# Optimization experiments

Measured on AMD Instinct MI355X. Metric: run time of the kernel, lower is better.

The kernel has to match this reference:

```python
import jax, jax.numpy as jnp
import numpy as np

N, E, H, EF, NG = 50000, 600000, 128, 4, 20
R_MIN, R_MAX = 0.0, 10.0

def setup_inputs() -> dict:
    key = jax.random.key(0)
    ks = jax.random.split(key, 20)
    s = lambda fi, fo: 1.0 / np.sqrt(fi)
    inp = {
        'h': jax.random.normal(ks[0], (N, H), jnp.float32),
        'x': jax.random.normal(ks[1], (N, 3), jnp.float32),
        'edge_index': jax.random.randint(ks[2], (2, E), 0, N, jnp.int32),
        'mask_ligand': jnp.ones((N,), jnp.float32),
        'edge_attr': jax.random.normal(ks[3], (E, EF), jnp.float32),
        # edge_mlp: Linear(2H+EF+NG,H) silu Linear(H,H) silu
        'We1': jax.random.normal(ks[4], (2*H+EF+NG, H), jnp.float32) * s(2*H+EF+NG, H),
        'be1': jnp.zeros((H,), jnp.float32),
        'We2': jax.random.normal(ks[5], (H, H), jnp.float32) * s(H, H),
        'be2': jnp.zeros((H,), jnp.float32),
        # edge_inf: Linear(H,1) sigmoid
        'Winf': jax.random.normal(ks[6], (H, 1), jnp.float32) * s(H, 1),
        'binf': jnp.zeros((1,), jnp.float32),
        # x_mlp: Linear(H,H) silu Linear(H,1,no bias, gain 0.001) tanh
        'Wx1': jax.random.normal(ks[7], (H, H), jnp.float32) * s(H, H),
        'bx1': jnp.zeros((H,), jnp.float32),
        'Wx2': jax.random.normal(ks[8], (H, 1), jnp.float32) * (0.001 * s(H, 1)),
        # node_mlp: Linear(2H,H) silu Linear(H,H)
        'Wn1': jax.random.normal(ks[9], (2*H, H), jnp.float32) * s(2*H, H),
        'bn1': jnp.zeros((H,), jnp.float32),
        'Wn2': jax.random.normal(ks[10], (H, H), jnp.float32) * s(H, H),
        'bn2': jnp.zeros((H,), jnp.float32),
    }
    return inp

def _gaussian_smearing(d):
    # d: [E,1] -> [E,NG]
    offset = jnp.linspace(R_MIN, R_MAX, NG, dtype=d.dtype)
    coeff = -0.5 / (offset[1] - offset[0]) ** 2
    return jnp.exp(coeff * (d - offset) ** 2)

def reference(h, x, edge_index, mask_ligand, edge_attr,
              We1, be1, We2, be2, Winf, binf, Wx1, bx1, Wx2,
              Wn1, bn1, Wn2, bn2):
    src, dst = edge_index[0], edge_index[1]
    hi, hj = h[dst], h[src]                      # [E,H]
    rel_x = x[dst] - x[src]                      # [E,3]
    d_sq = jnp.sum(rel_x ** 2, -1, keepdims=True)  # [E,1]
    d = jnp.sqrt(d_sq + 1e-8)
    d_feat = _gaussian_smearing(d)               # [E,NG]
    edge_feat = jnp.concatenate([d_feat, edge_attr], -1)
    inp = jnp.concatenate([hi, hj, edge_feat], -1)  # [E,2H+NG+EF]
    mij = jax.nn.silu(jax.nn.silu(inp @ We1 + be1) @ We2 + be2)  # [E,H]
    eij = jax.nn.sigmoid(mij @ Winf + binf)       # [E,1]
    n = h.shape[0]
    mi = jax.ops.segment_sum(mij * eij, dst, num_segments=n)  # [N,H]
    h_new = h + (jax.nn.silu(jnp.concatenate([mi, h], -1) @ Wn1 + bn1) @ Wn2 + bn2)
    gate = jnp.tanh(jax.nn.silu(mij @ Wx1 + bx1) @ Wx2)        # [E,1]
    delta_x = jax.ops.segment_sum(rel_x / (d + 1.0) * gate, dst, num_segments=n)
    x_new = x + delta_x * mask_ligand[:, None]
    return h_new, x_new
```

## Files before the change

### kernel.cpp

```cpp
#include <hip/hip_runtime.h>
#include <hip/hip_bf16.h>
#include <cstdint>

#define NN 50000
#define NE 600000
#define HD 128
#define NG 20
#define EF 4
#define K1 280
#define TILES (NE/64)
#define EGRID 512
#define ROWU 148
#define NTILE 782
#define SW(r) ((r) ^ (((r)>>3)&7))
#define EDW 12

typedef __attribute__((ext_vector_type(4))) float f32x4;
typedef __attribute__((ext_vector_type(8))) __bf16 bf16x8;
typedef __attribute__((ext_vector_type(4))) unsigned int u32x4;

__device__ __forceinline__ float fast_rcp(float x){ return __builtin_amdgcn_rcpf(x); }
__device__ __forceinline__ float silu_f(float x){ return x * fast_rcp(1.0f + __expf(-x)); }
__device__ __forceinline__ float sigmoid_f(float x){ return fast_rcp(1.0f + __expf(-x)); }
__device__ __forceinline__ float tanh_f(float x){ return 1.0f - 2.0f*fast_rcp(__expf(2.0f*x)+1.0f); }

__device__ __forceinline__ uint32_t pk2(float a, float b){
  uint32_t ua = __float_as_uint(a); ua += 0x7FFFu + ((ua>>16)&1u);
  uint32_t ub = __float_as_uint(b); ub += 0x7FFFu + ((ub>>16)&1u);
  return (ua>>16) | (ub & 0xFFFF0000u);
}
__device__ __forceinline__ uint16_t bfb(float a){
  uint32_t ua = __float_as_uint(a); ua += 0x7FFFu + ((ua>>16)&1u);
  return (uint16_t)(ua>>16);
}
__device__ __forceinline__ float bf2f(uint16_t b){ return __uint_as_float(((uint32_t)b)<<16); }
__device__ __forceinline__ f32x4 MF(u32x4 a, u32x4 b, f32x4 c){
  return __builtin_amdgcn_mfma_f32_16x16x32_bf16(
      __builtin_bit_cast(bf16x8, a), __builtin_bit_cast(bf16x8, b), c, 0, 0, 0);
}
__device__ __forceinline__ int mf_idx(int r, int c){
  return (((r>>4)*4 + (c>>5))*64 + SW(((((c>>4)&1)<<1) + ((c>>3)&1))*16 + (r&15)))*8 + (c&7);
}

__global__ void __launch_bounds__(256) h2bf_kernel(
    const float* __restrict__ h, uint32_t* __restrict__ hb)
{
  const size_t i = ((size_t)blockIdx.x*256 + threadIdx.x)*8;
  const float4 a = *reinterpret_cast<const float4*>(h + i);
  const float4 b = *reinterpret_cast<const float4*>(h + i + 4);
  u32x4 v = {pk2(a.x,a.y), pk2(a.z,a.w), pk2(b.x,b.y), pk2(b.z,b.w)};
  *reinterpret_cast<u32x4*>(hb + i/2) = v;
}

__global__ void __launch_bounds__(512) hist_kernel(
    const int* __restrict__ ei, int* __restrict__ cnt)
{
  const int e = blockIdx.x*512 + threadIdx.x;
  if (e < NE) atomicAdd(&cnt[ei[NE + e]], 1);
}

__global__ void __launch_bounds__(512) scanA_kernel(
    int* __restrict__ cur, int* __restrict__ bsums)
{
  __shared__ int s[512];
  const int tid = threadIdx.x;
  const int i = blockIdx.x*512 + tid;
  const int v = (i < NN) ? cur[i] : 0;
  s[tid] = v; __syncthreads();
  #pragma unroll
  for (int d = 1; d < 512; d <<= 1){
    const int t = (tid >= d) ? s[tid-d] : 0;
    __syncthreads();
    s[tid] += t;
    __syncthreads();
  }
  if (i < NN) cur[i] = s[tid] - v;
  if (tid == 511) bsums[blockIdx.x] = s[511];
}

__global__ void scanB_kernel(int* __restrict__ bsums)
{
  if (threadIdx.x == 0 && blockIdx.x == 0){
    int acc = 0;
    for (int b = 0; b < 98; ++b){ const int t = bsums[b]; bsums[b] = acc; acc += t; }
  }
}

__global__ void __launch_bounds__(512) scanC_kernel(
    int* __restrict__ cur, const int* __restrict__ bsums)
{
  const int i = blockIdx.x*512 + threadIdx.x;
  if (i < NN) cur[i] += bsums[blockIdx.x];
}

__global__ void __launch_bounds__(512) fill_kernel(
    const int* __restrict__ ei, int* __restrict__ cur, int* __restrict__ perm)
{
  const int e = blockIdx.x*512 + threadIdx.x;
  if (e < NE){
    const int p = atomicAdd(&cur[ei[NE + e]], 1);
    perm[p] = e;
  }
}

__global__ void __launch_bounds__(256) pregather_kernel(
    const int* __restrict__ ei, const float* __restrict__ x,
    const float* __restrict__ eattr, const int* __restrict__ perm,
    uint32_t* __restrict__ edata)
{
  const int i = blockIdx.x*256 + threadIdx.x;
  if (i >= NE) return;
  const int e = perm[i];
  const int sj = ei[e], dj = ei[NE + e];
  const float ax = x[dj*3+0]-x[sj*3+0];
  const float ay = x[dj*3+1]-x[sj*3+1];
  const float az = x[dj*3+2]-x[sj*3+2];
  const float dd = sqrtf(ax*ax + ay*ay + az*az + 1e-8f);
  const float4 e4 = *reinterpret_cast<const float4*>(eattr + (size_t)e*EF);
  uint32_t* dp = edata + (size_t)i*EDW;
  u32x4 v0 = {(uint32_t)sj, (uint32_t)dj, __float_as_uint(ax), __float_as_uint(ay)};
  u32x4 v1 = {__float_as_uint(az), __float_as_uint(dd), __float_as_uint(e4.x), __float_as_uint(e4.y)};
  u32x4 v2 = {__float_as_uint(e4.z), __float_as_uint(e4.w), 0u, 0u};
  *reinterpret_cast<u32x4*>(dp)     = v0;
  *reinterpret_cast<u32x4*>(dp + 4) = v1;
  *reinterpret_cast<u32x4*>(dp + 8) = v2;
}

#define EDGE_LDS_U32 (64*ROWU + 4096 + 4096 + 704)
#define EDGE_LDS_B (EDGE_LDS_U32*4)

__global__ void __launch_bounds__(512, 4) edge_red_kernel(
    const uint32_t* __restrict__ hb, const uint32_t* __restrict__ edata,
    const float* __restrict__ We1, const float* __restrict__ be1,
    const float* __restrict__ We2, const float* __restrict__ be2,
    const float* __restrict__ Winf, const float* __restrict__ binf,
    const float* __restrict__ Wx1, const float* __restrict__ bx1,
    const float* __restrict__ Wx2, float* __restrict__ out)
{
  extern __shared__ uint32_t smem[];
  uint32_t* s_inp = smem;
  uint16_t* t1f   = (uint16_t*)(smem + 64*ROWU);
  uint16_t* mf_   = (uint16_t*)(smem + 64*ROWU + 4096);
  uint32_t* tl    = smem + 64*ROWU + 8192;
  int*   s_dst    = (int*)tl;
  float* s_rel    = (float*)(tl+64);
  float* s_dist   = (float*)(tl+256);
  float* s_pe     = (float*)(tl+320);
  float* s_pg     = (float*)(tl+384);
  int*   s_udst   = (int*)(tl+448);
  int*   s_ustart = (int*)(tl+512);
  int*   s_Un     = (int*)(tl+580);

  const int tid = threadIdx.x;
  const int w = tid >> 6, l = tid & 63;
  const int lo = l & 15, hi = l >> 4;
  const int col = w*16 + lo;
  const int r8 = tid >> 3, p8 = tid & 7;
  const int ks2 = w >> 1;
  const int lp  = ((w&1)*2 + (lo>>3))*16 + 4*hi;
  const int jj  = lo & 7;
  const int lsw = SW(l);

  u32x4 B1[9], B2[4], B3[4];
  #pragma unroll
  for (int ks = 0; ks < 9; ++ks){
    float f[8];
    #pragma unroll
    for (int j = 0; j < 8; ++j){
      const int k = ks*32 + hi*8 + j;
      f[j] = (k < K1) ? We1[k*HD + col] : 0.0f;
    }
    B1[ks] = {pk2(f[0],f[1]), pk2(f[2],f[3]), pk2(f[4],f[5]), pk2(f[6],f[7])};
  }
  #pragma unroll
  for (int ks = 0; ks < 4; ++ks){
    float f2[8], f3[8];
    #pragma unroll
    for (int j = 0; j < 8; ++j){
      const int k = ks*32 + hi*8 + j;
      f2[j] = We2[k*HD + col];
      f3[j] = Wx1[k*HD + col];
    }
    B2[ks] = {pk2(f2[0],f2[1]), pk2(f2[2],f2[3]), pk2(f2[4],f2[5]), pk2(f2[6],f2[7])};
    B3[ks] = {pk2(f3[0],f3[1]), pk2(f3[2],f3[3]), pk2(f3[4],f3[5]), pk2(f3[6],f3[7])};
  }
  const float vbe1 = be1[col], vbe2 = be2[col], vbx1 = bx1[col];
  const float wi = Winf[col], wx = Wx2[col], vbinf = binf[0];
  const float SP = 10.0f/19.0f;
  const float CO = -0.5f/(SP*SP);

  for (int t = blockIdx.x; t < TILES; t += EGRID){
    const int ebase = t*64;
    __syncthreads();

    if (tid < 64){
      const uint32_t* ed = edata + (size_t)(ebase + tid)*EDW;
      const u32x4 w0 = *reinterpret_cast<const u32x4*>(ed);
      const u32x4 w1 = *reinterpret_cast<const u32x4*>(ed + 4);
      const u32x4 w2 = *reinterpret_cast<const u32x4*>(ed + 8);
      const int dj   = (int)w0.y;
      const float ax = __uint_as_float(w0.z);
      const float ay = __uint_as_float(w0.w);
      const float az = __uint_as_float(w1.x);
      const float dd = __uint_as_float(w1.y);
      s_dst[tid] = dj;
      s_rel[3*tid+0]=ax; s_rel[3*tid+1]=ay; s_rel[3*tid+2]=az;
      s_dist[tid]=dd; s_pe[tid]=0.0f; s_pg[tid]=0.0f;
      const int dprev = __shfl_up(dj, 1);
      const int isnew = (tid == 0) || (dj != dprev);
      const unsigned long long mball = __ballot(isnew);
      const int slot = __popcll(mball << (63 - tid)) - 1;
      if (isnew){ s_udst[slot] = dj; s_ustart[slot] = tid; }
      if (tid == 63){ s_Un[0] = slot + 1; s_ustart[slot + 1] = 64; }
      float g[24];
      #pragma unroll
      for (int j = 0; j < 20; ++j){ const float a = dd - j*SP; g[j] = __expf(CO*a*a); }
      g[20]=__uint_as_float(w1.z); g[21]=__uint_as_float(w1.w);
      g[22]=__uint_as_float(w2.x); g[23]=__uint_as_float(w2.y);
      uint32_t* gp = s_inp + tid*ROWU + 128;
      u32x4 g0v = {pk2(g[0],g[1]),  pk2(g[2],g[3]),  pk2(g[4],g[5]),  pk2(g[6],g[7])};
      u32x4 g1v = {pk2(g[8],g[9]),  pk2(g[10],g[11]),pk2(g[12],g[13]),pk2(g[14],g[15])};
      u32x4 g2v = {pk2(g[16],g[17]),pk2(g[18],g[19]),pk2(g[20],g[21]),pk2(g[22],g[23])};
      u32x4 g3v = {0,0,0,0};
      *reinterpret_cast<u32x4*>(gp)    = g0v;
      *reinterpret_cast<u32x4*>(gp+4)  = g1v;
      *reinterpret_cast<u32x4*>(gp+8)  = g2v;
      *reinterpret_cast<u32x4*>(gp+12) = g3v;
    }
    {
      const uint32_t node = edata[(size_t)(ebase + r8)*EDW + (p8 < 4 ? 1 : 0)];
      const uint32_t* hw = hb + (size_t)node*(HD/2) + (p8&3)*16;
      uint32_t* dp = s_inp + r8*ROWU + p8*16;
      #pragma unroll
      for (int q = 0; q < 4; ++q)
        *reinterpret_cast<u32x4*>(dp + 4*q) = *reinterpret_cast<const u32x4*>(hw + 4*q);
    }
    __syncthreads();

    #pragma unroll
    for (int Mt = 0; Mt < 4; ++Mt){
      const uint32_t* arow = s_inp + (Mt*16 + lo)*ROWU + hi*4;
      f32x4 acc = {0,0,0,0};
      #pragma unroll
      for (int ks = 0; ks < 9; ++ks)
        acc = MF(*reinterpret_cast<const u32x4*>(arow + ks*16), B1[ks], acc);
      #pragma unroll
      for (int reg = 0; reg < 4; ++reg)
        t1f[((Mt*4 + ks2)*64 + SW(lp+reg))*8 + jj] = bfb(silu_f(acc[reg] + vbe1));
    }
    __syncthreads();

    #pragma unroll
    for (int Mt = 0; Mt < 4; ++Mt){
      f32x4 acc = {0,0,0,0};
      #pragma unroll
      for (int ks = 0; ks < 4; ++ks)
        acc = MF(*reinterpret_cast<const u32x4*>(t1f + ((Mt*4+ks)*64 + lsw)*8), B2[ks], acc);
      float p[4];
      #pragma unroll
      for (int reg = 0; reg < 4; ++reg){
        const float m = silu_f(acc[reg] + vbe2);
        mf_[((Mt*4 + ks2)*64 + SW(lp+reg))*8 + jj] = bfb(m);
        p[reg] = m * wi;
      }
      #pragma unroll
      for (int msk = 1; msk < 16; msk <<= 1){
        #pragma unroll
        for (int reg = 0; reg < 4; ++reg) p[reg] += __shfl_xor(p[reg], msk);
      }
      if (lo == 0){
        #pragma unroll
        for (int reg = 0; reg < 4; ++reg) atomicAdd(&s_pe[Mt*16 + 4*hi + reg], p[reg]);
      }
    }
    __syncthreads();

    const int U = s_Un[0];
    for (int idx = tid; idx < U*HD; idx += 512){
      const int u = idx >> 7, c = idx & 127;
      const int r1 = s_ustart[u+1];
      float acc = 0.0f;
      for (int r = s_ustart[u]; r < r1; ++r){
        const float eij = sigmoid_f(s_pe[r] + vbinf);
        acc += bf2f(mf_[mf_idx(r, c)]) * eij;
      }
      atomicAdd(out + (size_t)s_udst[u]*HD + c, acc);
    }
    #pragma unroll
    for (int Mt = 0; Mt < 4; ++Mt){
      f32x4 acc = {0,0,0,0};
      #pragma unroll
      for (int ks = 0; ks < 4; ++ks)
        acc = MF(*reinterpret_cast<const u32x4*>(mf_ + ((Mt*4+ks)*64 + lsw)*8), B3[ks], acc);
      float p[4];
      #pragma unroll
      for (int reg = 0; reg < 4; ++reg)
        p[reg] = silu_f(acc[reg] + vbx1) * wx;
      #pragma unroll
      for (int msk = 1; msk < 16; msk <<= 1){
        #pragma unroll
        for (int reg = 0; reg < 4; ++reg) p[reg] += __shfl_xor(p[reg], msk);
      }
      if (lo == 0){
        #pragma unroll
        for (int reg = 0; reg < 4; ++reg) atomicAdd(&s_pg[Mt*16 + 4*hi + reg], p[reg]);
      }
    }
    __syncthreads();

    for (int idx = tid; idx < U*3; idx += 512){
      const int u = idx/3, cc = idx - 3*u;
      const int r1 = s_ustart[u+1];
      float acc = 0.0f;
      for (int r = s_ustart[u]; r < r1; ++r){
        const float gate = tanh_f(s_pg[r]);
        acc += s_rel[3*r+cc] * gate * fast_rcp(s_dist[r] + 1.0f);
      }
      atomicAdd(out + (size_t)NN*HD + (size_t)s_udst[u]*3 + cc, acc);
    }
  }
}

#define FB_LDS_U32 (64*ROWU + 4096 + 4096 + 448)
#define FB_LDS_B (FB_LDS_U32*4)

__global__ void __launch_bounds__(512, 4) edge_fb_kernel(
    const float* __restrict__ h, const float* __restrict__ x,
    const int* __restrict__ ei, const float* __restrict__ eattr,
    const float* __restrict__ We1, const float* __restrict__ be1,
    const float* __restrict__ We2, const float* __restrict__ be2,
    const float* __restrict__ Winf, const float* __restrict__ binf,
    const float* __restrict__ Wx1, const float* __restrict__ bx1,
    const float* __restrict__ Wx2, float* __restrict__ out)
{
  extern __shared__ uint32_t smem[];
  uint32_t* s_inp = smem;
  uint16_t* t1f   = (uint16_t*)(smem + 64*ROWU);
  uint16_t* mf_   = (uint16_t*)(smem + 64*ROWU + 4096);
  uint32_t* tl    = smem + 64*ROWU + 8192;
  int*   s_dst  = (int*)tl;
  float* s_rel  = (float*)(tl+64);
  float* s_dist = (float*)(tl+256);
  float* s_pe   = (float*)(tl+320);
  float* s_pg   = (float*)(tl+384);

  const int tid = threadIdx.x;
  const int w = tid >> 6, l = tid & 63;
  const int lo = l & 15, hi = l >> 4;
  const int col = w*16 + lo;
  const int r8 = tid >> 3, p8 = tid & 7;
  const int ks2 = w >> 1;
  const int lp  = ((w&1)*2 + (lo>>3))*16 + 4*hi;
  const int jj  = lo & 7;
  const int lsw = SW(l);

  u32x4 B1[9], B2[4], B3[4];
  #pragma unroll
  for (int ks = 0; ks < 9; ++ks){
    float f[8];
    #pragma unroll
    for (int j = 0; j < 8; ++j){
      const int k = ks*32 + hi*8 + j;
      f[j] = (k < K1) ? We1[k*HD + col] : 0.0f;
    }
    B1[ks] = {pk2(f[0],f[1]), pk2(f[2],f[3]), pk2(f[4],f[5]), pk2(f[6],f[7])};
  }
  #pragma unroll
  for (int ks = 0; ks < 4; ++ks){
    float f2[8], f3[8];
    #pragma unroll
    for (int j = 0; j < 8; ++j){
      const int k = ks*32 + hi*8 + j;
      f2[j] = We2[k*HD + col];
      f3[j] = Wx1[k*HD + col];
    }
    B2[ks] = {pk2(f2[0],f2[1]), pk2(f2[2],f2[3]), pk2(f2[4],f2[5]), pk2(f2[6],f2[7])};
    B3[ks] = {pk2(f3[0],f3[1]), pk2(f3[2],f3[3]), pk2(f3[4],f3[5]), pk2(f3[6],f3[7])};
  }
  const float vbe1 = be1[col], vbe2 = be2[col], vbx1 = bx1[col];
  const float wi = Winf[col], wx = Wx2[col], vbinf = binf[0];
  const float SP = 10.0f/19.0f;
  const float CO = -0.5f/(SP*SP);

  for (int t = blockIdx.x; t < TILES; t += EGRID){
    const int ebase = t*64;
    __syncthreads();
    if (tid < 64){
      const int sj = ei[ebase+tid], dj = ei[NE+ebase+tid];
      const float ax = x[dj*3+0]-x[sj*3+0];
      const float ay = x[dj*3+1]-x[sj*3+1];
      const float az = x[dj*3+2]-x[sj*3+2];
      const float dd = sqrtf(ax*ax + ay*ay + az*az + 1e-8f);
      s_dst[tid] = dj;
      s_rel[3*tid+0]=ax; s_rel[3*tid+1]=ay; s_rel[3*tid+2]=az;
      s_dist[tid]=dd; s_pe[tid]=0.0f; s_pg[tid]=0.0f;
      float g[24];
      #pragma unroll
      for (int j = 0; j < 20; ++j){ const float a = dd - j*SP; g[j] = __expf(CO*a*a); }
      const float4 e4 = *reinterpret_cast<const float4*>(eattr + (size_t)(ebase+tid)*EF);
      g[20]=e4.x; g[21]=e4.y; g[22]=e4.z; g[23]=e4.w;
      uint32_t* gp = s_inp + tid*ROWU + 128;
      u32x4 g0v = {pk2(g[0],g[1]),  pk2(g[2],g[3]),  pk2(g[4],g[5]),  pk2(g[6],g[7])};
      u32x4 g1v = {pk2(g[8],g[9]),  pk2(g[10],g[11]),pk2(g[12],g[13]),pk2(g[14],g[15])};
      u32x4 g2v = {pk2(g[16],g[17]),pk2(g[18],g[19]),pk2(g[20],g[21]),pk2(g[22],g[23])};
      u32x4 g3v = {0,0,0,0};
      *reinterpret_cast<u32x4*>(gp)    = g0v;
      *reinterpret_cast<u32x4*>(gp+4)  = g1v;
      *reinterpret_cast<u32x4*>(gp+8)  = g2v;
      *reinterpret_cast<u32x4*>(gp+12) = g3v;
    }
    {
      const int e = ebase + r8;
      const int node = (p8 < 4) ? ei[NE + e] : ei[e];
      const float* hp = h + (size_t)node*HD + (p8&3)*32;
      uint32_t* dp = s_inp + r8*ROWU + p8*16;
      #pragma unroll
      for (int q = 0; q < 4; ++q){
        const float4 va = *reinterpret_cast<const float4*>(hp + 8*q);
        const float4 vb = *reinterpret_cast<const float4*>(hp + 8*q + 4);
        u32x4 v = { pk2(va.x,va.y), pk2(va.z,va.w), pk2(vb.x,vb.y), pk2(vb.z,vb.w) };
        *reinterpret_cast<u32x4*>(dp + 4*q) = v;
      }
    }
    __syncthreads();

    #pragma unroll
    for (int Mt = 0; Mt < 4; ++Mt){
      const uint32_t* arow = s_inp + (Mt*16 + lo)*ROWU + hi*4;
      f32x4 acc = {0,0,0,0};
      #pragma unroll
      for (int ks = 0; ks < 9; ++ks)
        acc = MF(*reinterpret_cast<const u32x4*>(arow + ks*16), B1[ks], acc);
      #pragma unroll
      for (int reg = 0; reg < 4; ++reg)
        t1f[((Mt*4 + ks2)*64 + SW(lp+reg))*8 + jj] = bfb(silu_f(acc[reg] + vbe1));
    }
    __syncthreads();

    #pragma unroll
    for (int Mt = 0; Mt < 4; ++Mt){
      f32x4 acc = {0,0,0,0};
      #pragma unroll
      for (int ks = 0; ks < 4; ++ks)
        acc = MF(*reinterpret_cast<const u32x4*>(t1f + ((Mt*4+ks)*64 + lsw)*8), B2[ks], acc);
      float p[4];
      #pragma unroll
      for (int reg = 0; reg < 4; ++reg){
        const float m = silu_f(acc[reg] + vbe2);
        mf_[((Mt*4 + ks2)*64 + SW(lp+reg))*8 + jj] = bfb(m);
        p[reg] = m * wi;
      }
      #pragma unroll
      for (int msk = 1; msk < 16; msk <<= 1){
        #pragma unroll
        for (int reg = 0; reg < 4; ++reg) p[reg] += __shfl_xor(p[reg], msk);
      }
      if (lo == 0){
        #pragma unroll
        for (int reg = 0; reg < 4; ++reg) atomicAdd(&s_pe[Mt*16 + 4*hi + reg], p[reg]);
      }
    }
    __syncthreads();

    #pragma unroll
    for (int Mt = 0; Mt < 4; ++Mt){
      #pragma unroll
      for (int reg = 0; reg < 4; ++reg){
        const int r = Mt*16 + 4*hi + reg;
        const float eij = sigmoid_f(s_pe[r] + vbinf);
        const float m = bf2f(mf_[((Mt*4 + ks2)*64 + SW(lp+reg))*8 + jj]);
        atomicAdd(out + (size_t)s_dst[r]*HD + col, m*eij);
      }
    }
    #pragma unroll
    for (int Mt = 0; Mt < 4; ++Mt){
      f32x4 acc = {0,0,0,0};
      #pragma unroll
      for (int ks = 0; ks < 4; ++ks)
        acc = MF(*reinterpret_cast<const u32x4*>(mf_ + ((Mt*4+ks)*64 + lsw)*8), B3[ks], acc);
      float p[4];
      #pragma unroll
      for (int reg = 0; reg < 4; ++reg)
        p[reg] = silu_f(acc[reg] + vbx1) * wx;
      #pragma unroll
      for (int msk = 1; msk < 16; msk <<= 1){
        #pragma unroll
        for (int reg = 0; reg < 4; ++reg) p[reg] += __shfl_xor(p[reg], msk);
      }
      if (lo == 0){
        #pragma unroll
        for (int reg = 0; reg < 4; ++reg) atomicAdd(&s_pg[Mt*16 + 4*hi + reg], p[reg]);
      }
    }
    __syncthreads();

    if (tid < 192){
      const int er = tid/3, c = tid - 3*er;
      const float gate = tanh_f(s_pg[er]);
      const float sc = gate * fast_rcp(s_dist[er] + 1.0f);
      atomicAdd(out + (size_t)NN*HD + (size_t)s_dst[er]*3 + c, s_rel[3*er+c]*sc);
    }
  }
}

#define CROW 132

__global__ void __launch_bounds__(512, 4) node_kernel(
    const float* __restrict__ h, const float* __restrict__ x,
    const float* __restrict__ mask,
    const float* __restrict__ Wn1, const float* __restrict__ bn1,
    const float* __restrict__ Wn2, const float* __restrict__ bn2,
    float* __restrict__ out)
{
  __shared__ uint32_t s_cat[64*CROW];
  __shared__ __align__(16) uint16_t t1n[4*4*64*8];

  const int tid = threadIdx.x;
  const int w = tid >> 6, l = tid & 63;
  const int lo = l & 15, hi = l >> 4;
  const int col = w*16 + lo;

  u32x4 Bn1[8], Bn2[4];
  #pragma unroll
  for (int ks = 0; ks < 8; ++ks){
    float f[8];
    #pragma unroll
    for (int j = 0; j < 8; ++j) f[j] = Wn1[(ks*32 + hi*8 + j)*HD + col];
    Bn1[ks] = {pk2(f[0],f[1]), pk2(f[2],f[3]), pk2(f[4],f[5]), pk2(f[6],f[7])};
  }
  #pragma unroll
  for (int ks = 0; ks < 4; ++ks){
    float f[8];
    #pragma unroll
    for (int j = 0; j < 8; ++j) f[j] = Wn2[(ks*32 + hi*8 + j)*HD + col];
    Bn2[ks] = {pk2(f[0],f[1]), pk2(f[2],f[3]), pk2(f[4],f[5]), pk2(f[6],f[7])};
  }
  const float vbn1 = bn1[col], vbn2 = bn2[col];
  const int nbase = blockIdx.x*64;
  const int ks2 = w >> 1;
  const int lp  = ((w&1)*2 + (lo>>3))*16 + 4*hi;
  const int jj  = lo & 7;

  {
    const int r = tid >> 3, p = tid & 7;
    const int n = nbase + r;
    uint32_t* dp = s_cat + r*CROW + p*16;
    if (n < NN){
      const float* sp = (p < 4) ? (out + (size_t)n*HD + p*32)
                                : (h   + (size_t)n*HD + (p-4)*32);
      #pragma unroll
      for (int q = 0; q < 8; ++q){
        const float4 v = *reinterpret_cast<const float4*>(sp + 4*q);
        dp[2*q]   = pk2(v.x, v.y);
        dp[2*q+1] = pk2(v.z, v.w);
      }
    } else {
      #pragma unroll
      for (int q = 0; q < 16; ++q) dp[q] = 0u;
    }
  }
  __syncthreads();

  #pragma unroll
  for (int Mt = 0; Mt < 4; ++Mt){
    const uint32_t* arow = s_cat + (Mt*16 + lo)*CROW + hi*4;
    f32x4 acc = {0,0,0,0};
    #pragma unroll
    for (int ks = 0; ks < 8; ++ks)
      acc = MF(*reinterpret_cast<const u32x4*>(arow + ks*16), Bn1[ks], acc);
    uint16_t* tp = t1n + ((Mt*4 + ks2)*64 + lp)*8 + jj;
    #pragma unroll
    for (int reg = 0; reg < 4; ++reg)
      tp[reg*8] = bfb(silu_f(acc[reg] + vbn1));
  }
  __syncthreads();

  #pragma unroll
  for (int Mt = 0; Mt < 4; ++Mt){
    f32x4 acc = {0,0,0,0};
    #pragma unroll
    for (int ks = 0; ks < 4; ++ks)
      acc = MF(*reinterpret_cast<const u32x4*>(t1n + ((Mt*4+ks)*64 + l)*8), Bn2[ks], acc);
    #pragma unroll
    for (int reg = 0; reg < 4; ++reg){
      const int n = nbase + Mt*16 + 4*hi + reg;
      if (n < NN)
        out[(size_t)n*HD + col] = h[(size_t)n*HD + col] + acc[reg] + vbn2;
    }
  }

  if (tid < 192){
    const int r = tid/3, c = tid - 3*r;
    const int n = nbase + r;
    if (n < NN){
      const size_t ix = (size_t)NN*HD + (size_t)n*3 + c;
      out[ix] = x[(size_t)n*3 + c] + out[ix]*mask[n];
    }
  }
}

extern "C" void kernel_launch(void* const* d_in, const int* in_sizes, int n_in,
                              void* d_out, int out_size, void* d_ws, size_t ws_size,
                              hipStream_t stream) {
  (void)in_sizes; (void)n_in;
  const float* h    = (const float*)d_in[0];
  const float* x    = (const float*)d_in[1];
  const int*   ei   = (const int*)  d_in[2];
  const float* mask = (const float*)d_in[3];
  const float* ea   = (const float*)d_in[4];
  const float* We1  = (const float*)d_in[5];
  const float* be1  = (const float*)d_in[6];
  const float* We2  = (const float*)d_in[7];
  const float* be2  = (const float*)d_in[8];
  const float* Winf = (const float*)d_in[9];
  const float* binf = (const float*)d_in[10];
  const float* Wx1  = (const float*)d_in[11];
  const float* bx1  = (const float*)d_in[12];
  const float* Wx2  = (const float*)d_in[13];
  const float* Wn1  = (const float*)d_in[14];
  const float* bn1  = (const float*)d_in[15];
  const float* Wn2  = (const float*)d_in[16];
  const float* bn2  = (const float*)d_in[17];
  float* out = (float*)d_out;

  uint32_t* hb    = (uint32_t*)d_ws;
  int* cursor     = (int*)d_ws + 3200000;
  int* perm       = (int*)d_ws + 3250000;
  int* bsums      = (int*)d_ws + 3850000;
  uint32_t* edata = (uint32_t*)d_ws + 3850128;
  const size_t need = (size_t)(3850128 + (size_t)NE*EDW) * 4;
  const bool use_red = ws_size >= need;

  hipFuncSetAttribute(reinterpret_cast<const void*>(edge_red_kernel),
                      hipFuncAttributeMaxDynamicSharedMemorySize, EDGE_LDS_B);
  hipFuncSetAttribute(reinterpret_cast<const void*>(edge_fb_kernel),
                      hipFuncAttributeMaxDynamicSharedMemorySize, FB_LDS_B);

  hipMemsetAsync(d_out, 0, (size_t)out_size * sizeof(float), stream);

  if (use_red){
    hipMemsetAsync(cursor, 0, (size_t)NN*4, stream);
    h2bf_kernel<<<3125, 256, 0, stream>>>(h, hb);
    hist_kernel<<<1172, 512, 0, stream>>>(ei, cursor);
    scanA_kernel<<<98, 512, 0, stream>>>(cursor, bsums);
    scanB_kernel<<<1, 64, 0, stream>>>(bsums);
    scanC_kernel<<<98, 512, 0, stream>>>(cursor, bsums);
    fill_kernel<<<1172, 512, 0, stream>>>(ei, cursor, perm);
    pregather_kernel<<<2344, 256, 0, stream>>>(ei, x, ea, perm, edata);
    edge_red_kernel<<<EGRID, 512, EDGE_LDS_B, stream>>>(
        hb, edata, We1, be1, We2, be2, Winf, binf, Wx1, bx1, Wx2, out);
  } else {
    edge_fb_kernel<<<EGRID, 512, FB_LDS_B, stream>>>(
        h, x, ei, ea, We1, be1, We2, be2, Winf, binf, Wx1, bx1, Wx2, out);
  }
  node_kernel<<<NTILE, 512, 0, stream>>>(
      h, x, mask, Wn1, bn1, Wn2, bn2, out);
}
```

Baseline: 487.9 us.

## Double-buffer edge tile metadata and prefetch next tile's inputs during compute

The edge reduction kernel now loads the next tile's gathered node features and per-edge metadata while the current tile's second and third MLP stages run. The per-edge scalars sit in two ping-pong buffers so one loop-top barrier goes away. The sigmoid and gate factors are computed once per edge into shared memory instead of inside every segment loop, and the mf_ index math is simplified. This costs extra LDS, and the prefetch into s_inp has to be correctly ordered against the first GEMM's reads.

Measured after the change: 454.3 us. 6.9% less time.

```diff
diff --git a/kernel.cpp b/kernel.cpp
--- a/kernel.cpp
+++ b/kernel.cpp
@@ -14,6 +14,7 @@
 #define NTILE 782
 #define SW(r) ((r) ^ (((r)>>3)&7))
 #define EDW 12
+#define TLW 520
 
 typedef __attribute__((ext_vector_type(4))) float f32x4;
 typedef __attribute__((ext_vector_type(8))) __bf16 bf16x8;
@@ -37,9 +38,6 @@
 __device__ __forceinline__ f32x4 MF(u32x4 a, u32x4 b, f32x4 c){
   return __builtin_amdgcn_mfma_f32_16x16x32_bf16(
       __builtin_bit_cast(bf16x8, a), __builtin_bit_cast(bf16x8, b), c, 0, 0, 0);
-}
-__device__ __forceinline__ int mf_idx(int r, int c){
-  return (((r>>4)*4 + (c>>5))*64 + SW(((((c>>4)&1)<<1) + ((c>>3)&1))*16 + (r&15)))*8 + (c&7);
 }
 
 __global__ void __launch_bounds__(256) h2bf_kernel(
@@ -126,7 +124,7 @@
   *reinterpret_cast<u32x4*>(dp + 8) = v2;
 }
 
-#define EDGE_LDS_U32 (64*ROWU + 4096 + 4096 + 704)
+#define EDGE_LDS_U32 (64*ROWU + 4096 + 4096 + 2*TLW + 64)
 #define EDGE_LDS_B (EDGE_LDS_U32*4)
 
 __global__ void __launch_bounds__(512, 4) edge_red_kernel(
@@ -141,15 +139,8 @@
   uint32_t* s_inp = smem;
   uint16_t* t1f   = (uint16_t*)(smem + 64*ROWU);
   uint16_t* mf_   = (uint16_t*)(smem + 64*ROWU + 4096);
-  uint32_t* tl    = smem + 64*ROWU + 8192;
-  int*   s_dst    = (int*)tl;
-  float* s_rel    = (float*)(tl+64);
-  float* s_dist   = (float*)(tl+256);
-  float* s_pe     = (float*)(tl+320);
-  float* s_pg     = (float*)(tl+384);
-  int*   s_udst   = (int*)(tl+448);
-  int*   s_ustart = (int*)(tl+512);
-  int*   s_Un     = (int*)(tl+580);
+  uint32_t* tlb   = smem + 64*ROWU + 8192;
+  float*    s_eij = (float*)(smem + 64*ROWU + 8192 + 2*TLW);
 
   const int tid = threadIdx.x;
   const int w = tid >> 6, l = tid & 63;
@@ -189,12 +180,23 @@
   const float SP = 10.0f/19.0f;
   const float CO = -0.5f/(SP*SP);
 
-  for (int t = blockIdx.x; t < TILES; t += EGRID){
-    const int ebase = t*64;
-    __syncthreads();
-
+  auto stage = [&](int nb, uint32_t* tq){
+    {
+      const uint32_t node = edata[(size_t)(nb + r8)*EDW + (p8 < 4 ? 1 : 0)];
+      const uint32_t* hw = hb + (size_t)node*(HD/2) + (p8&3)*16;
+      uint32_t* dp = s_inp + r8*ROWU + p8*16;
+      #pragma unroll
+      for (int q = 0; q < 4; ++q)
+        *reinterpret_cast<u32x4*>(dp + 4*q) = *reinterpret_cast<const u32x4*>(hw + 4*q);
+    }
     if (tid < 64){
-      const uint32_t* ed = edata + (size_t)(ebase + tid)*EDW;
+      float* q_rel  = (float*)(tq);
+      float* q_dist = (float*)(tq+192);
+      float* q_pe   = (float*)(tq+256);
+      float* q_pg   = (float*)(tq+320);
+      int*   q_udst = (int*)(tq+384);
+      int*   q_ust  = (int*)(tq+448);
+      const uint32_t* ed = edata + (size_t)(nb + tid)*EDW;
       const u32x4 w0 = *reinterpret_cast<const u32x4*>(ed);
       const u32x4 w1 = *reinterpret_cast<const u32x4*>(ed + 4);
       const u32x4 w2 = *reinterpret_cast<const u32x4*>(ed + 8);
@@ -203,15 +205,14 @@
       const float ay = __uint_as_float(w0.w);
       const float az = __uint_as_float(w1.x);
       const float dd = __uint_as_float(w1.y);
-      s_dst[tid] = dj;
-      s_rel[3*tid+0]=ax; s_rel[3*tid+1]=ay; s_rel[3*tid+2]=az;
-      s_dist[tid]=dd; s_pe[tid]=0.0f; s_pg[tid]=0.0f;
+      q_rel[3*tid+0]=ax; q_rel[3*tid+1]=ay; q_rel[3*tid+2]=az;
+      q_dist[tid]=dd; q_pe[tid]=0.0f; q_pg[tid]=0.0f;
       const int dprev = __shfl_up(dj, 1);
       const int isnew = (tid == 0) || (dj != dprev);
       const unsigned long long mball = __ballot(isnew);
       const int slot = __popcll(mball << (63 - tid)) - 1;
-      if (isnew){ s_udst[slot] = dj; s_ustart[slot] = tid; }
-      if (tid == 63){ s_Un[0] = slot + 1; s_ustart[slot + 1] = 64; }
+      if (isnew){ q_udst[slot] = dj; q_ust[slot] = tid; }
+      if (tid == 63){ q_ust[slot + 1] = 64; q_ust[65] = slot + 1; }
       float g[24];
       #pragma unroll
       for (int j = 0; j < 20; ++j){ const float a = dd - j*SP; g[j] = __expf(CO*a*a); }
@@ -227,15 +228,20 @@
       *reinterpret_cast<u32x4*>(gp+8)  = g2v;
       *reinterpret_cast<u32x4*>(gp+12) = g3v;
     }
-    {
-      const uint32_t node = edata[(size_t)(ebase + r8)*EDW + (p8 < 4 ? 1 : 0)];
-      const uint32_t* hw = hb + (size_t)node*(HD/2) + (p8&3)*16;
-      uint32_t* dp = s_inp + r8*ROWU + p8*16;
-      #pragma unroll
-      for (int q = 0; q < 4; ++q)
-        *reinterpret_cast<u32x4*>(dp + 4*q) = *reinterpret_cast<const u32x4*>(hw + 4*q);
-    }
-    __syncthreads();
+  };
+
+  stage(blockIdx.x*64, tlb);
+  __syncthreads();
+
+  int p = 0;
+  for (int t = blockIdx.x; t < TILES; t += EGRID, p ^= 1){
+    uint32_t* tlp = tlb + p*TLW;
+    float* s_rel  = (float*)(tlp);
+    float* s_dist = (float*)(tlp+192);
+    float* s_pe   = (float*)(tlp+256);
+    float* s_pg   = (float*)(tlp+320);
+    int*   s_udst = (int*)(tlp+384);
+    int*   s_ust  = (int*)(tlp+448);
 
     #pragma unroll
     for (int Mt = 0; Mt < 4; ++Mt){
@@ -250,39 +256,46 @@
     }
     __syncthreads();
 
+    if (t + EGRID < TILES) stage((t + EGRID)*64, tlb + (p^1)*TLW);
+
     #pragma unroll
     for (int Mt = 0; Mt < 4; ++Mt){
       f32x4 acc = {0,0,0,0};
       #pragma unroll
       for (int ks = 0; ks < 4; ++ks)
         acc = MF(*reinterpret_cast<const u32x4*>(t1f + ((Mt*4+ks)*64 + lsw)*8), B2[ks], acc);
-      float p[4];
+      float pq[4];
       #pragma unroll
       for (int reg = 0; reg < 4; ++reg){
         const float m = silu_f(acc[reg] + vbe2);
         mf_[((Mt*4 + ks2)*64 + SW(lp+reg))*8 + jj] = bfb(m);
-        p[reg] = m * wi;
+        pq[reg] = m * wi;
       }
       #pragma unroll
       for (int msk = 1; msk < 16; msk <<= 1){
         #pragma unroll
-        for (int reg = 0; reg < 4; ++reg) p[reg] += __shfl_xor(p[reg], msk);
+        for (int reg = 0; reg < 4; ++reg) pq[reg] += __shfl_xor(pq[reg], msk);
       }
       if (lo == 0){
         #pragma unroll
-        for (int reg = 0; reg < 4; ++reg) atomicAdd(&s_pe[Mt*16 + 4*hi + reg], p[reg]);
-      }
-    }
-    __syncthreads();
-
-    const int U = s_Un[0];
+        for (int reg = 0; reg < 4; ++reg) atomicAdd(&s_pe[Mt*16 + 4*hi + reg], pq[reg]);
+      }
+    }
+    __syncthreads();
+
+    s_eij[l] = sigmoid_f(s_pe[l] + vbinf);
+    const int U = s_ust[65];
+
     for (int idx = tid; idx < U*HD; idx += 512){
       const int u = idx >> 7, c = idx & 127;
-      const int r1 = s_ustart[u+1];
+      const int r0 = s_ust[u], r1 = s_ust[u+1];
+      const int cb = c >> 5, cc = ((c>>4)&1)*2 + ((c>>3)&1);
+      const int base = (cb*64 + cc*16)*8 + (c & 7);
+      const int x2 = cc*2;
       float acc = 0.0f;
-      for (int r = s_ustart[u]; r < r1; ++r){
-        const float eij = sigmoid_f(s_pe[r] + vbinf);
-        acc += bf2f(mf_[mf_idx(r, c)]) * eij;
+      for (int r = r0; r < r1; ++r){
+        const int mix = (r>>4)*2048 + base + (((r&15) ^ ((x2 + ((r>>3)&1))&7))<<3);
+        acc += bf2f(mf_[mix]) * s_eij[r];
       }
       atomicAdd(out + (size_t)s_udst[u]*HD + c, acc);
     }
@@ -292,31 +305,31 @@
       #pragma unroll
       for (int ks = 0; ks < 4; ++ks)
         acc = MF(*reinterpret_cast<const u32x4*>(mf_ + ((Mt*4+ks)*64 + lsw)*8), B3[ks], acc);
-      float p[4];
+      float pq[4];
       #pragma unroll
       for (int reg = 0; reg < 4; ++reg)
-        p[reg] = silu_f(acc[reg] + vbx1) * wx;
+        pq[reg] = silu_f(acc[reg] + vbx1) * wx;
       #pragma unroll
       for (int msk = 1; msk < 16; msk <<= 1){
         #pragma unroll
-        for (int reg = 0; reg < 4; ++reg) p[reg] += __shfl_xor(p[reg], msk);
+        for (int reg = 0; reg < 4; ++reg) pq[reg] += __shfl_xor(pq[reg], msk);
       }
       if (lo == 0){
         #pragma unroll
-        for (int reg = 0; reg < 4; ++reg) atomicAdd(&s_pg[Mt*16 + 4*hi + reg], p[reg]);
-      }
-    }
-    __syncthreads();
-
-    for (int idx = tid; idx < U*3; idx += 512){
-      const int u = idx/3, cc = idx - 3*u;
-      const int r1 = s_ustart[u+1];
-      float acc = 0.0f;
-      for (int r = s_ustart[u]; r < r1; ++r){
-        const float gate = tanh_f(s_pg[r]);
-        acc += s_rel[3*r+cc] * gate * fast_rcp(s_dist[r] + 1.0f);
-      }
-      atomicAdd(out + (size_t)NN*HD + (size_t)s_udst[u]*3 + cc, acc);
+        for (int reg = 0; reg < 4; ++reg) atomicAdd(&s_pg[Mt*16 + 4*hi + reg], pq[reg]);
+      }
+    }
+    __syncthreads();
+
+    if (tid < 64){
+      s_eij[tid] = tanh_f(s_pg[tid]) * fast_rcp(s_dist[tid] + 1.0f);
+      for (int idx = tid; idx < U*3; idx += 64){
+        const int u = idx/3, cc2 = idx - 3*u;
+        float acc = 0.0f;
+        for (int r = s_ust[u]; r < s_ust[u+1]; ++r)
+          acc += s_rel[3*r+cc2] * s_eij[r];
+        atomicAdd(out + (size_t)NN*HD + (size_t)s_udst[u]*3 + cc2, acc);
+      }
     }
   }
 }
@@ -443,21 +456,21 @@
       #pragma unroll
       for (int ks = 0; ks < 4; ++ks)
         acc = MF(*reinterpret_cast<const u32x4*>(t1f + ((Mt*4+ks)*64 + lsw)*8), B2[ks], acc);
-      float p[4];
+      float pq[4];
       #pragma unroll
       for (int reg = 0; reg < 4; ++reg){
         const float m = silu_f(acc[reg] + vbe2);
         mf_[((Mt*4 + ks2)*64 + SW(lp+reg))*8 + jj] = bfb(m);
-        p[reg] = m * wi;
+        pq[reg] = m * wi;
       }
       #pragma unroll
       for (int msk = 1; msk < 16; msk <<= 1){
         #pragma unroll
-        for (int reg = 0; reg < 4; ++reg) p[reg] += __shfl_xor(p[reg], msk);
+        for (int reg = 0; reg < 4; ++reg) pq[reg] += __shfl_xor(pq[reg], msk);
       }
       if (lo == 0){
         #pragma unroll
-        for (int reg = 0; reg < 4; ++reg) atomicAdd(&s_pe[Mt*16 + 4*hi + reg], p[reg]);
+        for (int reg = 0; reg < 4; ++reg) atomicAdd(&s_pe[Mt*16 + 4*hi + reg], pq[reg]);
       }
     }
     __syncthreads();
@@ -478,18 +491,18 @@
       #pragma unroll
       for (int ks = 0; ks < 4; ++ks)
         acc = MF(*reinterpret_cast<const u32x4*>(mf_ + ((Mt*4+ks)*64 + lsw)*8), B3[ks], acc);
-      float p[4];
+      float pq[4];
       #pragma unroll
       for (int reg = 0; reg < 4; ++reg)
-        p[reg] = silu_f(acc[reg] + vbx1) * wx;
+        pq[reg] = silu_f(acc[reg] + vbx1) * wx;
       #pragma unroll
       for (int msk = 1; msk < 16; msk <<= 1){
         #pragma unroll
-        for (int reg = 0; reg < 4; ++reg) p[reg] += __shfl_xor(p[reg], msk);
+        for (int reg = 0; reg < 4; ++reg) pq[reg] += __shfl_xor(pq[reg], msk);
       }
       if (lo == 0){
         #pragma unroll
-        for (int reg = 0; reg < 4; ++reg) atomicAdd(&s_pg[Mt*16 + 4*hi + reg], p[reg]);
+        for (int reg = 0; reg < 4; ++reg) atomicAdd(&s_pg[Mt*16 + 4*hi + reg], pq[reg]);
       }
     }
     __syncthreads();
```
